# Kernel tuning notes

Measured on AMD Instinct MI355X. Metric: run time of the kernel, lower is better.

The kernel has to match this reference:

```python
import jax, jax.numpy as jnp
import numpy as np

N_CONVEX = 256
N_FREE = 256
HIDDEN = [1024, 1024, 1024, 1024]
BATCH = 8192
# mono lists: first 4 cols increasing, next 4 decreasing, rest unconstrained
MONO = [1.0] * 4 + [-1.0] * 4

def _sign_vec(n_in):
    s = np.zeros((n_in,), dtype=np.float32)
    s[: len(MONO)] = np.asarray(MONO, dtype=np.float32)
    return jnp.asarray(s)

SIGN_C = _sign_vec(N_CONVEX)
SIGN_F = _sign_vec(N_FREE)

def apply_col_monotone(raw_w, sign):
    # raw_w: [h, n_in]; sign: [n_in] in {+1,-1,0}; 0 -> leave column as raw
    pos = jax.nn.softplus(raw_w)
    return jnp.where(sign != 0.0, sign * pos, raw_w)

def setup_inputs() -> dict:
    key = jax.random.key(0)
    ks = jax.random.split(key, 8)
    L = len(HIDDEN)
    h = HIDDEN[0]
    xc = jax.random.normal(ks[0], (BATCH, N_CONVEX), dtype=jnp.float32)
    xf = jax.random.normal(ks[1], (BATCH, N_FREE), dtype=jnp.float32)
    Wc_w = jax.random.normal(ks[2], (L, h, N_CONVEX), dtype=jnp.float32) * 0.1
    Wc_b = jnp.zeros((L, h), dtype=jnp.float32)
    Wu_w = jax.random.normal(ks[3], (L, h, N_FREE), dtype=jnp.float32) * 0.1
    Wu_b = jnp.zeros((L, h), dtype=jnp.float32)
    Wut_w = jax.random.normal(ks[4], (L, h, N_FREE), dtype=jnp.float32) * 0.1
    Wut_b = jnp.zeros((L, h), dtype=jnp.float32)
    # raw_U[i] used for layers i=1..L-1; layer 0 has no recurrence
    raw_U = jax.random.normal(ks[5], (L - 1, h, h), dtype=jnp.float32) * 0.1
    return {"xc": xc, "xf": xf, "Wc_w": Wc_w, "Wc_b": Wc_b, "Wu_w": Wu_w,
            "Wu_b": Wu_b, "Wut_w": Wut_w, "Wut_b": Wut_b, "raw_U": raw_U}

def reference(xc, xf, Wc_w, Wc_b, Wu_w, Wu_b, Wut_w, Wut_b, raw_U):
    relu = jax.nn.relu
    z = None
    for i in range(len(HIDDEN)):
        # u_{i+1} = act(linear(xf, mono(Wu_tilde)))
        Wut = apply_col_monotone(Wut_w[i], SIGN_F)
        u = relu(xf @ Wut.T + Wut_b[i])
        # convex-input path
        Wc = apply_col_monotone(Wc_w[i], SIGN_C)
        agg = xc @ Wc.T + Wc_b[i]
        # free-input path
        Wu = apply_col_monotone(Wu_w[i], SIGN_F)
        agg = agg + xf @ Wu.T + Wu_b[i]
        # recurrent nonnegative U path
        if i > 0:
            agg = agg + z @ jax.nn.softplus(raw_U[i - 1]).T
        agg = agg + u
        z = relu(agg)
    return z
```

## Files before the change

### kernel.cpp

```cpp
#include <hip/hip_runtime.h>
#include <hip/hip_bf16.h>
#include <stdint.h>

typedef __attribute__((ext_vector_type(8))) short short8;
typedef __attribute__((ext_vector_type(4))) float f32x4;

__device__ __forceinline__ float softplus_f(float x) {
    float e = __expf(-fabsf(x));
    return fmaxf(x, 0.f) + __logf(1.f + e);
}

__global__ void xform_all(const float* __restrict__ xc, const float* __restrict__ xf,
                          const float* __restrict__ Wc_w, const float* __restrict__ Wu_w,
                          const float* __restrict__ Wut_w, const float* __restrict__ raw_U,
                          short* __restrict__ xc_bf, short* __restrict__ xf_bf,
                          short* __restrict__ Wc_bf, short* __restrict__ Wu_bf,
                          short* __restrict__ Wut_bf, short* __restrict__ U_bf)
{
    int j = blockIdx.x * blockDim.x + threadIdx.x;
    const float* src; short* dst; int mode;
    if (j < 524288)                    { src = xc;    dst = xc_bf;  mode = 0; }
    else if ((j -= 524288) < 524288)   { src = xf;    dst = xf_bf;  mode = 0; }
    else if ((j -= 524288) < 262144)   { src = Wc_w;  dst = Wc_bf;  mode = 1; }
    else if ((j -= 262144) < 262144)   { src = Wu_w;  dst = Wu_bf;  mode = 1; }
    else if ((j -= 262144) < 262144)   { src = Wut_w; dst = Wut_bf; mode = 1; }
    else                               { j -= 262144; src = raw_U;  dst = U_bf;  mode = 2; }
    float4 v = reinterpret_cast<const float4*>(src)[j];
    float r[4] = {v.x, v.y, v.z, v.w};
    int base = j << 2;
#pragma unroll
    for (int e = 0; e < 4; ++e) {
        float x = r[e];
        float y = x;
        if (mode == 2) {
            y = softplus_f(x);
        } else if (mode == 1) {
            int col = (base + e) & 255;
            if (col < 8) {
                float s = softplus_f(x);
                y = (col < 4) ? s : -s;
            }
        }
        ((__hip_bfloat16*)dst)[base + e] = __float2bfloat16(y);
    }
}

#define GLOAD16(src, dst)                                                                  \
    __builtin_amdgcn_global_load_lds((const __attribute__((address_space(1))) void*)(src), \
                                     (__attribute__((address_space(3))) void*)(dst), 16, 0, 0)

#define DSREAD(dst, addr, off_lit) \
    asm volatile("ds_read_b128 %0, %1 offset:" #off_lit : "=v"(dst) : "v"(addr))

__device__ __forceinline__ uint32_t lds_addr32(const short* p) {
    return (uint32_t)(uintptr_t)(const __attribute__((address_space(3))) short*)p;
}

template<bool HAS_U, bool WRITE_F32>
__global__ __launch_bounds__(256, 2)
void icnn_layer_kernel(const short* __restrict__ xc, const short* __restrict__ xf,
                       const short* __restrict__ zin,
                       const short* __restrict__ Wc, const short* __restrict__ Wu,
                       const short* __restrict__ Wut, const short* __restrict__ U,
                       const float* __restrict__ bc, const float* __restrict__ bu,
                       const float* __restrict__ but,
                       __hip_bfloat16* __restrict__ zout, float* __restrict__ fout)
{
    __shared__ short lds_s[4][128 * 64];
    const int t_ = threadIdx.x;
    const int lane = t_ & 63;
    const int wid = t_ >> 6;
    const int wr = wid >> 1, wc = wid & 1;
    const int l15 = lane & 15, l4 = lane >> 4;
    const int swz = l15 & 7;
    const int brow = blockIdx.x * 128;
    const int bcol = blockIdx.y * 128;

    constexpr int NSTEP = HAS_U ? 28 : 12;

    f32x4 acc[4][4];
#pragma unroll
    for (int m = 0; m < 4; ++m)
#pragma unroll
        for (int n = 0; n < 4; ++n) acc[m][n] = (f32x4){0.f, 0.f, 0.f, 0.f};

    float bt[4];
#pragma unroll
    for (int n = 0; n < 4; ++n) bt[n] = but[bcol + wc * 64 + n * 16 + l15];

    auto seg = [&](int s, const short*& A, int& lsa, const short*& B, int& lsb, int& k0) {
        if (s < 4)       { A = xf;  lsa = 8;  B = Wut; lsb = 8;  k0 = s * 64; }
        else if (s < 8)  { A = xc;  lsa = 8;  B = Wc;  lsb = 8;  k0 = (s - 4) * 64; }
        else if (s < 12) { A = xf;  lsa = 8;  B = Wu;  lsb = 8;  k0 = (s - 8) * 64; }
        else             { A = zin; lsa = 10; B = U;   lsb = 10; k0 = (s - 12) * 64; }
    };

    auto stage = [&](short* Ad, short* Bd, int s) {
        const short *Ag, *Bg; int lsa, lsb, k0;
        seg(s, Ag, lsa, Bg, lsb, k0);
#pragma unroll
        for (int it = 0; it < 4; ++it) {
            int c = it * 256 + t_;
            int row = c >> 3;
            int js = (c & 7) ^ (row & 7);
            GLOAD16(Ag + (((size_t)(brow + row)) << lsa) + k0 + js * 8, Ad + c * 8);
        }
#pragma unroll
        for (int it = 0; it < 4; ++it) {
            int c = it * 256 + t_;
            int row = c >> 3;
            int js = (c & 7) ^ (row & 7);
            GLOAD16(Bg + (((size_t)(bcol + row)) << lsb) + k0 + js * 8, Bd + c * 8);
        }
    };

    auto tile = [&](const short* As, const short* Bs, short* An, short* Bn, int t) {
        asm volatile("s_waitcnt vmcnt(0)" ::: "memory");
        __builtin_amdgcn_s_barrier();

        if (t + 1 < NSTEP) stage(An, Bn, t + 1);
        __builtin_amdgcn_sched_barrier(0);

        const uint32_t abase = lds_addr32(As) + ((uint32_t)(wr * 64 + l15) << 7);
        const uint32_t bbase = lds_addr32(Bs) + ((uint32_t)(wc * 64 + l15) << 7);
        const uint32_t a0 = abase + (uint32_t)((l4 ^ swz) << 4);
        const uint32_t a1 = abase + (uint32_t)(((4 + l4) ^ swz) << 4);
        const uint32_t b0 = bbase + (uint32_t)((l4 ^ swz) << 4);
        const uint32_t b1 = bbase + (uint32_t)(((4 + l4) ^ swz) << 4);

        short8 a[2][4], b[2][4];
        DSREAD(a[0][0], a0, 0);    DSREAD(a[0][1], a0, 2048);
        DSREAD(a[0][2], a0, 4096); DSREAD(a[0][3], a0, 6144);
        DSREAD(b[0][0], b0, 0);    DSREAD(b[0][1], b0, 2048);
        DSREAD(b[0][2], b0, 4096); DSREAD(b[0][3], b0, 6144);
        DSREAD(a[1][0], a1, 0);    DSREAD(a[1][1], a1, 2048);
        DSREAD(a[1][2], a1, 4096); DSREAD(a[1][3], a1, 6144);
        DSREAD(b[1][0], b1, 0);    DSREAD(b[1][1], b1, 2048);
        DSREAD(b[1][2], b1, 4096); DSREAD(b[1][3], b1, 6144);

        asm volatile("s_waitcnt lgkmcnt(8)" ::: "memory");
        __builtin_amdgcn_sched_barrier(0);
        __builtin_amdgcn_s_setprio(1);
#pragma unroll
        for (int m = 0; m < 4; ++m)
#pragma unroll
            for (int n = 0; n < 4; ++n)
                acc[m][n] = __builtin_amdgcn_mfma_f32_16x16x32_bf16(a[0][m], b[0][n], acc[m][n], 0, 0, 0);
        asm volatile("s_waitcnt lgkmcnt(0)" ::: "memory");
        __builtin_amdgcn_sched_barrier(0);
#pragma unroll
        for (int m = 0; m < 4; ++m)
#pragma unroll
            for (int n = 0; n < 4; ++n)
                acc[m][n] = __builtin_amdgcn_mfma_f32_16x16x32_bf16(a[1][m], b[1][n], acc[m][n], 0, 0, 0);
        __builtin_amdgcn_s_setprio(0);

        if (t == 3) {
#pragma unroll
            for (int n = 0; n < 4; ++n)
#pragma unroll
                for (int m = 0; m < 4; ++m)
#pragma unroll
                    for (int v = 0; v < 4; ++v)
                        acc[m][n][v] = fmaxf(acc[m][n][v] + bt[n], 0.f);
        }
    };

    stage(lds_s[0], lds_s[2], 0);

    for (int i = 0; i < NSTEP / 2; ++i) {
        tile(lds_s[0], lds_s[2], lds_s[1], lds_s[3], 2 * i);
        tile(lds_s[1], lds_s[3], lds_s[0], lds_s[2], 2 * i + 1);
    }

    float bb[4];
#pragma unroll
    for (int n = 0; n < 4; ++n) {
        int col = bcol + wc * 64 + n * 16 + l15;
        bb[n] = bc[col] + bu[col];
    }

    if constexpr (WRITE_F32) {
#pragma unroll
        for (int n = 0; n < 4; ++n) {
            int col = bcol + wc * 64 + n * 16 + l15;
#pragma unroll
            for (int m = 0; m < 4; ++m) {
                int row = brow + wr * 64 + m * 16 + l4 * 4;
#pragma unroll
                for (int v = 0; v < 4; ++v)
                    fout[(size_t)(row + v) * 1024 + col] = fmaxf(acc[m][n][v] + bb[n], 0.f);
            }
        }
    } else {
        __syncthreads();
        float* fs = (float*)&lds_s[0][0];
#pragma unroll
        for (int n = 0; n < 4; ++n) {
            int col = wc * 64 + n * 16 + l15;
#pragma unroll
            for (int m = 0; m < 4; ++m) {
                int row = wr * 64 + m * 16 + l4 * 4;
#pragma unroll
                for (int v = 0; v < 4; ++v)
                    fs[(row + v) * 128 + col] = fmaxf(acc[m][n][v] + bb[n], 0.f);
            }
        }
        __syncthreads();
        const int rrow = t_ >> 5;
        const int rcol = (t_ & 31) * 4;
#pragma unroll
        for (int p = 0; p < 16; ++p) {
            int row = p * 8 + rrow;
            float4 v4 = *(const float4*)&fs[row * 128 + rcol];
            ushort4 o;
            o.x = __bfloat16_as_ushort(__float2bfloat16(v4.x));
            o.y = __bfloat16_as_ushort(__float2bfloat16(v4.y));
            o.z = __bfloat16_as_ushort(__float2bfloat16(v4.z));
            o.w = __bfloat16_as_ushort(__float2bfloat16(v4.w));
            *(ushort4*)&zout[(size_t)(brow + row) * 1024 + bcol + rcol] = o;
        }
    }
}

extern "C" void kernel_launch(void* const* d_in, const int* in_sizes, int n_in,
                              void* d_out, int out_size, void* d_ws, size_t ws_size,
                              hipStream_t stream)
{
    const float* xc    = (const float*)d_in[0];
    const float* xf    = (const float*)d_in[1];
    const float* Wc_w  = (const float*)d_in[2];
    const float* Wc_b  = (const float*)d_in[3];
    const float* Wu_w  = (const float*)d_in[4];
    const float* Wu_b  = (const float*)d_in[5];
    const float* Wut_w = (const float*)d_in[6];
    const float* Wut_b = (const float*)d_in[7];
    const float* raw_U = (const float*)d_in[8];

    short* p = (short*)d_ws;
    short* xc_bf  = p; p += 8192 * 256;
    short* xf_bf  = p; p += 8192 * 256;
    short* Wc_bf  = p; p += 4 * 1024 * 256;
    short* Wu_bf  = p; p += 4 * 1024 * 256;
    short* Wut_bf = p; p += 4 * 1024 * 256;
    short* U_bf   = p; p += 3 * 1024 * 1024;
    short* z_a    = p; p += 8192 * 1024;
    short* z_b = (short*)d_out;

    xform_all<<<dim3(10240), dim3(256), 0, stream>>>(
        xc, xf, Wc_w, Wu_w, Wut_w, raw_U,
        xc_bf, xf_bf, Wc_bf, Wu_bf, Wut_bf, U_bf);

    dim3 tb(256);
    dim3 grid(8192 / 128, 1024 / 128);
    const int WS = 1024 * 256;
    const int US = 1024 * 1024;

    icnn_layer_kernel<false, false><<<grid, tb, 0, stream>>>(
        xc_bf, xf_bf, nullptr, Wc_bf, Wu_bf, Wut_bf, nullptr,
        Wc_b, Wu_b, Wut_b, (__hip_bfloat16*)z_a, nullptr);
    icnn_layer_kernel<true, false><<<grid, tb, 0, stream>>>(
        xc_bf, xf_bf, z_a, Wc_bf + WS, Wu_bf + WS, Wut_bf + WS, U_bf,
        Wc_b + 1024, Wu_b + 1024, Wut_b + 1024, (__hip_bfloat16*)z_b, nullptr);
    icnn_layer_kernel<true, false><<<grid, tb, 0, stream>>>(
        xc_bf, xf_bf, z_b, Wc_bf + 2 * WS, Wu_bf + 2 * WS, Wut_bf + 2 * WS, U_bf + US,
        Wc_b + 2048, Wu_b + 2048, Wut_b + 2048, (__hip_bfloat16*)z_a, nullptr);
    icnn_layer_kernel<true, true><<<grid, tb, 0, stream>>>(
        xc_bf, xf_bf, z_a, Wc_bf + 3 * WS, Wu_bf + 3 * WS, Wut_bf + 3 * WS, U_bf + 2 * US,
        Wc_b + 3072, Wu_b + 3072, Wut_b + 3072, nullptr, (float*)d_out);
}
```

Before: 125.8 us.

## Load B operand fragments directly from global into registers, halving LDS

Instead of staging the weight (B) tile through LDS, each wave now loads its B fragments straight from global memory into registers, double-buffered across steps, while A stays in LDS. LDS use drops from 64KB to 32KB per block, which could allow more blocks per CU, and the epilogue is split into two half-width passes to fit the smaller buffer. In exchange the B loads are uncoalesced 16-byte reads shared redundantly by the two waves in each column, register pressure rises from the extra double buffer, and the vmcnt(0) wait now also covers those global loads.

After: 238.4 us. 1.9x slower.

```diff
diff --git a/kernel.cpp b/kernel.cpp
--- a/kernel.cpp
+++ b/kernel.cpp
@@ -66,7 +66,7 @@
                        const float* __restrict__ but,
                        __hip_bfloat16* __restrict__ zout, float* __restrict__ fout)
 {
-    __shared__ short lds_s[4][128 * 64];
+    __shared__ short lds_s[2][128 * 64];
     const int t_ = threadIdx.x;
     const int lane = t_ & 63;
     const int wid = t_ >> 6;
@@ -95,7 +95,7 @@
         else             { A = zin; lsa = 10; B = U;   lsb = 10; k0 = (s - 12) * 64; }
     };
 
-    auto stage = [&](short* Ad, short* Bd, int s) {
+    auto stageA = [&](short* Ad, int s) {
         const short *Ag, *Bg; int lsa, lsb, k0;
         seg(s, Ag, lsa, Bg, lsb, k0);
 #pragma unroll
@@ -105,54 +105,50 @@
             int js = (c & 7) ^ (row & 7);
             GLOAD16(Ag + (((size_t)(brow + row)) << lsa) + k0 + js * 8, Ad + c * 8);
         }
-#pragma unroll
-        for (int it = 0; it < 4; ++it) {
-            int c = it * 256 + t_;
-            int row = c >> 3;
-            int js = (c & 7) ^ (row & 7);
-            GLOAD16(Bg + (((size_t)(bcol + row)) << lsb) + k0 + js * 8, Bd + c * 8);
-        }
-    };
-
-    auto tile = [&](const short* As, const short* Bs, short* An, short* Bn, int t) {
+    };
+
+    auto loadB = [&](short8 (&B)[2][4], int s) {
+        const short *Ag, *Bg; int lsa, lsb, k0;
+        seg(s, Ag, lsa, Bg, lsb, k0);
+        const short* base = Bg + (((size_t)(bcol + wc * 64 + l15)) << lsb) + k0 + l4 * 8;
+#pragma unroll
+        for (int kk = 0; kk < 2; ++kk)
+#pragma unroll
+            for (int n = 0; n < 4; ++n)
+                B[kk][n] = *(const short8*)(base + (((size_t)(n * 16)) << lsb) + kk * 32);
+    };
+
+    auto tile = [&](const short* As, short* An, short8 (&Bc)[2][4], short8 (&Bn)[2][4], int t) {
         asm volatile("s_waitcnt vmcnt(0)" ::: "memory");
         __builtin_amdgcn_s_barrier();
 
-        if (t + 1 < NSTEP) stage(An, Bn, t + 1);
+        if (t + 1 < NSTEP) { stageA(An, t + 1); loadB(Bn, t + 1); }
         __builtin_amdgcn_sched_barrier(0);
 
         const uint32_t abase = lds_addr32(As) + ((uint32_t)(wr * 64 + l15) << 7);
-        const uint32_t bbase = lds_addr32(Bs) + ((uint32_t)(wc * 64 + l15) << 7);
         const uint32_t a0 = abase + (uint32_t)((l4 ^ swz) << 4);
         const uint32_t a1 = abase + (uint32_t)(((4 + l4) ^ swz) << 4);
-        const uint32_t b0 = bbase + (uint32_t)((l4 ^ swz) << 4);
-        const uint32_t b1 = bbase + (uint32_t)(((4 + l4) ^ swz) << 4);
-
-        short8 a[2][4], b[2][4];
+        short8 a[2][4];
         DSREAD(a[0][0], a0, 0);    DSREAD(a[0][1], a0, 2048);
         DSREAD(a[0][2], a0, 4096); DSREAD(a[0][3], a0, 6144);
-        DSREAD(b[0][0], b0, 0);    DSREAD(b[0][1], b0, 2048);
-        DSREAD(b[0][2], b0, 4096); DSREAD(b[0][3], b0, 6144);
         DSREAD(a[1][0], a1, 0);    DSREAD(a[1][1], a1, 2048);
         DSREAD(a[1][2], a1, 4096); DSREAD(a[1][3], a1, 6144);
-        DSREAD(b[1][0], b1, 0);    DSREAD(b[1][1], b1, 2048);
-        DSREAD(b[1][2], b1, 4096); DSREAD(b[1][3], b1, 6144);
-
-        asm volatile("s_waitcnt lgkmcnt(8)" ::: "memory");
+
+        asm volatile("s_waitcnt lgkmcnt(4)" ::: "memory");
         __builtin_amdgcn_sched_barrier(0);
         __builtin_amdgcn_s_setprio(1);
 #pragma unroll
         for (int m = 0; m < 4; ++m)
 #pragma unroll
             for (int n = 0; n < 4; ++n)
-                acc[m][n] = __builtin_amdgcn_mfma_f32_16x16x32_bf16(a[0][m], b[0][n], acc[m][n], 0, 0, 0);
+                acc[m][n] = __builtin_amdgcn_mfma_f32_16x16x32_bf16(a[0][m], Bc[0][n], acc[m][n], 0, 0, 0);
         asm volatile("s_waitcnt lgkmcnt(0)" ::: "memory");
         __builtin_amdgcn_sched_barrier(0);
 #pragma unroll
         for (int m = 0; m < 4; ++m)
 #pragma unroll
             for (int n = 0; n < 4; ++n)
-                acc[m][n] = __builtin_amdgcn_mfma_f32_16x16x32_bf16(a[1][m], b[1][n], acc[m][n], 0, 0, 0);
+                acc[m][n] = __builtin_amdgcn_mfma_f32_16x16x32_bf16(a[1][m], Bc[1][n], acc[m][n], 0, 0, 0);
         __builtin_amdgcn_s_setprio(0);
 
         if (t == 3) {
@@ -166,11 +162,13 @@
         }
     };
 
-    stage(lds_s[0], lds_s[2], 0);
+    short8 B0[2][4], B1[2][4];
+    stageA(lds_s[0], 0);
+    loadB(B0, 0);
 
     for (int i = 0; i < NSTEP / 2; ++i) {
-        tile(lds_s[0], lds_s[2], lds_s[1], lds_s[3], 2 * i);
-        tile(lds_s[1], lds_s[3], lds_s[0], lds_s[2], 2 * i + 1);
+        tile(lds_s[0], lds_s[1], B0, B1, 2 * i);
+        tile(lds_s[1], lds_s[0], B1, B0, 2 * i + 1);
     }
 
     float bb[4];
@@ -193,32 +191,36 @@
             }
         }
     } else {
-        __syncthreads();
         float* fs = (float*)&lds_s[0][0];
 #pragma unroll
-        for (int n = 0; n < 4; ++n) {
-            int col = wc * 64 + n * 16 + l15;
-#pragma unroll
-            for (int m = 0; m < 4; ++m) {
-                int row = wr * 64 + m * 16 + l4 * 4;
-#pragma unroll
-                for (int v = 0; v < 4; ++v)
-                    fs[(row + v) * 128 + col] = fmaxf(acc[m][n][v] + bb[n], 0.f);
-            }
-        }
-        __syncthreads();
-        const int rrow = t_ >> 5;
-        const int rcol = (t_ & 31) * 4;
-#pragma unroll
-        for (int p = 0; p < 16; ++p) {
-            int row = p * 8 + rrow;
-            float4 v4 = *(const float4*)&fs[row * 128 + rcol];
-            ushort4 o;
-            o.x = __bfloat16_as_ushort(__float2bfloat16(v4.x));
-            o.y = __bfloat16_as_ushort(__float2bfloat16(v4.y));
-            o.z = __bfloat16_as_ushort(__float2bfloat16(v4.z));
-            o.w = __bfloat16_as_ushort(__float2bfloat16(v4.w));
-            *(ushort4*)&zout[(size_t)(brow + row) * 1024 + bcol + rcol] = o;
+        for (int h = 0; h < 2; ++h) {
+            __syncthreads();
+            if (wc == h) {
+#pragma unroll
+                for (int n = 0; n < 4; ++n) {
+                    int col = n * 16 + l15;
+#pragma unroll
+                    for (int m = 0; m < 4; ++m) {
+                        int row = wr * 64 + m * 16 + l4 * 4;
+#pragma unroll
+                        for (int v = 0; v < 4; ++v)
+                            fs[(row + v) * 64 + col] = fmaxf(acc[m][n][v] + bb[n], 0.f);
+                    }
+                }
+            }
+            __syncthreads();
+#pragma unroll
+            for (int p = 0; p < 8; ++p) {
+                int row = p * 16 + (t_ >> 4);
+                int col = (t_ & 15) * 4;
+                float4 v4 = *(const float4*)&fs[row * 64 + col];
+                ushort4 o;
+                o.x = __bfloat16_as_ushort(__float2bfloat16(v4.x));
+                o.y = __bfloat16_as_ushort(__float2bfloat16(v4.y));
+                o.z = __bfloat16_as_ushort(__float2bfloat16(v4.z));
+                o.w = __bfloat16_as_ushort(__float2bfloat16(v4.w));
+                *(ushort4*)&zout[(size_t)(brow + row) * 1024 + bcol + h * 64 + col] = o;
+            }
         }
     }
 }
```
